# Kernel optimization log

Measured on AMD Instinct MI355X. Metric: run time of the kernel, lower is better.

## Reference

```python
import jax, jax.numpy as jnp
import numpy as np

B, S, D = 4, 2048, 1024
H = 16
HD = D // H


def setup_inputs() -> dict:
    key = jax.random.key(0)
    ks = jax.random.split(key, 5)
    scale = 0.02
    return {
        "x": jax.random.normal(ks[0], (B, S, D), dtype=jnp.float32),
        "wq": jax.random.normal(ks[1], (D, D), dtype=jnp.float32) * scale,
        "wk": jax.random.normal(ks[2], (D, D), dtype=jnp.float32) * scale,
        "wv": jax.random.normal(ks[3], (D, D), dtype=jnp.float32) * scale,
        "wo": jax.random.normal(ks[4], (D, D), dtype=jnp.float32) * scale,
    }


def reference(x, wq, wk, wv, wo):
    b, s, _ = x.shape
    # project and split heads: [b, h, s, hd]
    def proj(w):
        return jnp.einsum('bsd,de->bse', x, w).reshape(b, s, H, HD).transpose(0, 2, 1, 3)
    q, k, v = proj(wq), proj(wk), proj(wv)
    scores = jnp.einsum('bhqd,bhkd->bhqk', q, k)
    causal = jnp.tril(jnp.ones((s, s), dtype=bool))  # True = keep
    scores = jnp.where(causal, scores, -jnp.inf)
    attn = jax.nn.softmax(scores / jnp.sqrt(jnp.float32(HD)), axis=-1)
    ctx = jnp.einsum('bhqk,bhkd->bhqd', attn, v)
    ctx = ctx.transpose(0, 2, 1, 3).reshape(b, s, D)
    return jnp.einsum('bsd,de->bse', ctx, wo)
```

## Files before the change

kernel.cpp:

```cpp
#include <hip/hip_runtime.h>

#define S_LEN 2048
#define D_DIM 1024
#define NH    16
#define HD    64
#define BATCH 4
#define M_ROWS 8192

typedef __attribute__((ext_vector_type(8))) short bf16x8;
typedef __attribute__((ext_vector_type(4))) float f32x4;
typedef __attribute__((ext_vector_type(8))) unsigned short u16x8;

__device__ __forceinline__ unsigned short f2bf(float f) {
    unsigned u = __builtin_bit_cast(unsigned, f);
    u = (u + 0x7fffu + ((u >> 16) & 1u)) >> 16;
    return (unsigned short)u;
}
__device__ __forceinline__ unsigned pack2(float a, float b) {
    unsigned ua = __builtin_bit_cast(unsigned, a);
    unsigned ub = __builtin_bit_cast(unsigned, b);
    return ((ua + 0x8000u) >> 16) | ((ub + 0x8000u) & 0xffff0000u);
}

__device__ __forceinline__ void gload16(const void* g, void* l) {
    __builtin_amdgcn_global_load_lds((const __attribute__((address_space(1))) unsigned*)g,
                                     (__attribute__((address_space(3))) unsigned*)l,
                                     16, 0, 0);
}

__global__ __launch_bounds__(256) void prep_k(const float* __restrict__ x,
                                              const float* __restrict__ w0, const float* __restrict__ w1,
                                              const float* __restrict__ w2, const float* __restrict__ w3,
                                              unsigned short* __restrict__ xbf,
                                              unsigned short* __restrict__ o0, unsigned short* __restrict__ o1,
                                              unsigned short* __restrict__ o2, unsigned short* __restrict__ o3) {
    __shared__ float sT[64][65];
    const int t = threadIdx.x;
    if (blockIdx.x < 4096) {
        size_t i = (size_t)blockIdx.x * 256 + t;
        const float4* xf = (const float4*)x;
        float4 a = xf[2 * i], b = xf[2 * i + 1];
        u16x8 v;
        v[0] = f2bf(a.x); v[1] = f2bf(a.y); v[2] = f2bf(a.z); v[3] = f2bf(a.w);
        v[4] = f2bf(b.x); v[5] = f2bf(b.y); v[6] = f2bf(b.z); v[7] = f2bf(b.w);
        *(u16x8*)(xbf + i * 8) = v;
        return;
    }
    const int wb = blockIdx.x - 4096;
    const int z = wb >> 8;
    const float* w; unsigned short* o;
    switch (z) {
        case 0: w = w0; o = o0; break;
        case 1: w = w1; o = o1; break;
        case 2: w = w2; o = o2; break;
        default: w = w3; o = o3; break;
    }
    const float sc = (z == 0) ? 0.18033688011112042f : 1.0f;
    const int n0 = (wb & 15) * 64, k0 = ((wb >> 4) & 15) * 64;
    const int r = t >> 4, cq = t & 15;
#pragma unroll
    for (int it = 0; it < 4; ++it) {
        int k = r + it * 16;
        float4 v = *(const float4*)&w[(size_t)(k0 + k) * D_DIM + n0 + cq * 4];
        sT[k][cq * 4 + 0] = v.x; sT[k][cq * 4 + 1] = v.y;
        sT[k][cq * 4 + 2] = v.z; sT[k][cq * 4 + 3] = v.w;
    }
    __syncthreads();
    const int n = t >> 2, ch = t & 3;
    union { unsigned short s[8]; uint4 v; } p0, p1;
#pragma unroll
    for (int j = 0; j < 8; ++j) p0.s[j] = f2bf(sT[ch * 16 + j][n] * sc);
#pragma unroll
    for (int j = 0; j < 8; ++j) p1.s[j] = f2bf(sT[ch * 16 + 8 + j][n] * sc);
    *(uint4*)&o[(size_t)(n0 + n) * D_DIM + k0 + ch * 16]     = p0.v;
    *(uint4*)&o[(size_t)(n0 + n) * D_DIM + k0 + ch * 16 + 8] = p1.v;
}

__device__ __forceinline__ void gemm_core(const unsigned short* __restrict__ A,
                                          const unsigned short* __restrict__ Bt,
                                          unsigned short* sA, unsigned short* sB,
                                          int m0, int n0, int t, f32x4 acc[4][4])
{
    const int lane = t & 63, w = t >> 6;
    const int mm = lane & 15, quad = lane >> 4;
    const int wm = w >> 1, wn = w & 1;

    for (int k0 = 0; k0 < D_DIM; k0 += 64) {
        __syncthreads();
#pragma unroll
        for (int it = 0; it < 4; ++it) {
            int idx = t + it * 256;
            int m = idx >> 3, j = idx & 7;
            int g = j ^ (m & 7);
            gload16(A  + ((size_t)(m0 + m) * D_DIM + k0 + g * 8), (void*)&sA[idx * 8]);
            gload16(Bt + ((size_t)(n0 + m) * D_DIM + k0 + g * 8), (void*)&sB[idx * 8]);
        }
        __syncthreads();

#pragma unroll
        for (int kk = 0; kk < 2; ++kk) {
            bf16x8 af[4], bfr[4];
#pragma unroll
            for (int mi = 0; mi < 4; ++mi) {
                int m = wm * 64 + mi * 16 + mm;
                int slot = (kk * 4 + quad) ^ (m & 7);
                af[mi] = *(const bf16x8*)&sA[m * 64 + slot * 8];
            }
#pragma unroll
            for (int ni = 0; ni < 4; ++ni) {
                int n = wn * 64 + ni * 16 + mm;
                int slot = (kk * 4 + quad) ^ (n & 7);
                bfr[ni] = *(const bf16x8*)&sB[n * 64 + slot * 8];
            }
#pragma unroll
            for (int mi = 0; mi < 4; ++mi)
#pragma unroll
                for (int ni = 0; ni < 4; ++ni)
                    acc[mi][ni] = __builtin_amdgcn_mfma_f32_16x16x32_bf16(af[mi], bfr[ni], acc[mi][ni], 0, 0, 0);
        }
    }
}

__global__ __launch_bounds__(256) void gemmqkv_k(const unsigned short* __restrict__ A,
                                                 const unsigned short* __restrict__ Bt,
                                                 unsigned short* __restrict__ qb,
                                                 unsigned short* __restrict__ kb,
                                                 unsigned short* __restrict__ vt)
{
    __shared__ unsigned short sA[128 * 64];
    __shared__ unsigned short sB[128 * 64];
    const int t = threadIdx.x;
    const int lane = t & 63, w = t >> 6;
    const int mm = lane & 15, quad = lane >> 4;
    const int wm = w >> 1, wn = w & 1;
    const int m0 = blockIdx.y * 128, n0 = blockIdx.x * 128;

    f32x4 acc[4][4];
#pragma unroll
    for (int i = 0; i < 4; ++i)
#pragma unroll
        for (int j = 0; j < 4; ++j) acc[i][j] = (f32x4){0.f, 0.f, 0.f, 0.f};

    gemm_core(A, Bt, sA, sB, m0, n0, t, acc);

    const int widx = n0 >> 10;
    if (widx == 2) {
#pragma unroll
        for (int mi = 0; mi < 4; ++mi) {
            int rglob = m0 + wm * 64 + mi * 16 + quad * 4;
            int bb = rglob >> 11, ss = rglob & (S_LEN - 1);
#pragma unroll
            for (int ni = 0; ni < 4; ++ni) {
                int c = (n0 & 1023) + wn * 64 + ni * 16 + mm;
                int h = c >> 6, hd = c & 63;
                union { unsigned short s[4]; unsigned long long ll; } pk;
#pragma unroll
                for (int r = 0; r < 4; ++r) pk.s[r] = f2bf(acc[mi][ni][r]);
                *(unsigned long long*)&vt[((size_t)(bb * NH + h) * HD + hd) * S_LEN + ss] = pk.ll;
            }
        }
    } else {
        unsigned short* outp = widx ? kb : qb;
        const int nl0 = n0 & 1023;
#pragma unroll
        for (int mi = 0; mi < 4; ++mi)
#pragma unroll
            for (int ni = 0; ni < 4; ++ni)
#pragma unroll
                for (int r = 0; r < 4; ++r)
                    outp[(size_t)(m0 + wm * 64 + mi * 16 + quad * 4 + r) * D_DIM +
                         nl0 + wn * 64 + ni * 16 + mm] = f2bf(acc[mi][ni][r]);
    }
}

__global__ __launch_bounds__(256) void gemmo_k(const unsigned short* __restrict__ A,
                                               const unsigned short* __restrict__ Bt,
                                               float* __restrict__ C)
{
    __shared__ unsigned short sA[128 * 64];
    __shared__ unsigned short sB[128 * 64];
    const int t = threadIdx.x;
    const int lane = t & 63, w = t >> 6;
    const int mm = lane & 15, quad = lane >> 4;
    const int wm = w >> 1, wn = w & 1;
    const int m0 = blockIdx.y * 128, n0 = blockIdx.x * 128;

    f32x4 acc[4][4];
#pragma unroll
    for (int i = 0; i < 4; ++i)
#pragma unroll
        for (int j = 0; j < 4; ++j) acc[i][j] = (f32x4){0.f, 0.f, 0.f, 0.f};

    gemm_core(A, Bt, sA, sB, m0, n0, t, acc);

#pragma unroll
    for (int mi = 0; mi < 4; ++mi)
#pragma unroll
        for (int ni = 0; ni < 4; ++ni)
#pragma unroll
            for (int r = 0; r < 4; ++r)
                C[(size_t)(m0 + wm * 64 + mi * 16 + quad * 4 + r) * D_DIM +
                  n0 + wn * 64 + ni * 16 + mm] = acc[mi][ni][r];
}

__global__ __launch_bounds__(512, 4) void attn_k(const unsigned short* __restrict__ Q,
                                                 const unsigned short* __restrict__ K,
                                                 const unsigned short* __restrict__ Vt,
                                                 unsigned short* __restrict__ ctx)
{
    __shared__ unsigned short sK [2][64 * 64];
    __shared__ unsigned short sVT[2][64 * 64];
    __shared__ unsigned short sP [128 * 64];
    const int t = threadIdx.x;
    const int lane = t & 63, w = t >> 6;
    const int mm = lane & 15, quad = lane >> 4;
    const int pair = blockIdx.x, bh = blockIdx.y;
    const int b = bh >> 4, hh = bh & 15;
    const size_t rowbase = (size_t)b * S_LEN;
    const int coff = hh * HD;
    const unsigned short* Vh = Vt + (size_t)bh * HD * S_LEN;

    const int sc_ = t >> 3, sj = t & 7;
    const int sgk = sj ^ (sc_ & 7);

    u16x8 onesu;
#pragma unroll
    for (int j = 0; j < 8; ++j) onesu[j] = 0x3F80;
    const bf16x8 ones = __builtin_bit_cast(bf16x8, onesu);

    for (int sidx = 0; sidx < 2; ++sidx) {
        const int qt = sidx ? (15 - pair) : pair;
        const int q0 = qt * 128;

        bf16x8 qf[2];
#pragma unroll
        for (int kk = 0; kk < 2; ++kk)
            qf[kk] = *(const bf16x8*)(Q + (rowbase + q0 + w * 16 + mm) * D_DIM
                                        + coff + kk * 32 + quad * 8);
        f32x4 o[4], lacc;
        lacc = (f32x4){0.f, 0.f, 0.f, 0.f};
#pragma unroll
        for (int hf = 0; hf < 4; ++hf) o[hf] = (f32x4){0.f, 0.f, 0.f, 0.f};

        const int nkt = 2 * qt + 2;
        const int qr = q0 + w * 16 + mm;
        const int qrmax = q0 + w * 16 + 15;
        const int m = w * 16 + mm;

        gload16(K  + (rowbase + sc_) * D_DIM + coff + sgk * 8, (void*)&sK[0][t * 8]);
        gload16(Vh + (size_t)sc_ * S_LEN + sgk * 8,            (void*)&sVT[0][t * 8]);

        for (int kt = 0; kt < nkt; ++kt) {
            const int buf = kt & 1;
            __syncthreads();
            if (kt + 1 < nkt) {
                const int k1 = (kt + 1) * 64;
                gload16(K  + (rowbase + k1 + sc_) * D_DIM + coff + sgk * 8,
                        (void*)&sK[1 - buf][t * 8]);
                gload16(Vh + (size_t)sc_ * S_LEN + k1 + sgk * 8,
                        (void*)&sVT[1 - buf][t * 8]);
            }
            const int k0 = kt * 64;
            if (k0 > qrmax) continue;

            f32x4 sacc[4];
#pragma unroll
            for (int kf = 0; kf < 4; ++kf) sacc[kf] = (f32x4){0.f, 0.f, 0.f, 0.f};
#pragma unroll
            for (int kk = 0; kk < 2; ++kk) {
                bf16x8 ak[4];
#pragma unroll
                for (int kf = 0; kf < 4; ++kf) {
                    int key = kf * 16 + mm;
                    int slot = (kk * 4 + quad) ^ (key & 7);
                    ak[kf] = *(const bf16x8*)&sK[buf][key * 64 + slot * 8];
                }
#pragma unroll
                for (int kf = 0; kf < 4; ++kf)
                    sacc[kf] = __builtin_amdgcn_mfma_f32_16x16x32_bf16(ak[kf], qf[kk], sacc[kf], 0, 0, 0);
            }

            const bool needmask = (k0 + 63) > (q0 + w * 16);
#pragma unroll
            for (int kf = 0; kf < 4; ++kf) {
                float p[4];
#pragma unroll
                for (int r = 0; r < 4; ++r) {
                    p[r] = __builtin_amdgcn_exp2f(sacc[kf][r]);
                    if (needmask && (k0 + kf * 16 + quad * 4 + r) > qr) p[r] = 0.f;
                }
                unsigned lo = pack2(p[0], p[1]), hi = pack2(p[2], p[3]);
                int slot = (kf * 2 + (quad >> 1)) ^ (m & 7);
                *(unsigned long long*)&sP[m * 64 + slot * 8 + (quad & 1) * 4] =
                    ((unsigned long long)hi << 32) | lo;
            }

#pragma unroll
            for (int kk = 0; kk < 2; ++kk) {
                bf16x8 pf, vf[4];
                {
                    int slot = (kk * 4 + quad) ^ (m & 7);
                    pf = *(const bf16x8*)&sP[m * 64 + slot * 8];
                }
#pragma unroll
                for (int hf = 0; hf < 4; ++hf) {
                    int hd = hf * 16 + mm;
                    int slot = (kk * 4 + quad) ^ (hd & 7);
                    vf[hf] = *(const bf16x8*)&sVT[buf][hd * 64 + slot * 8];
                }
                lacc = __builtin_amdgcn_mfma_f32_16x16x32_bf16(pf, ones, lacc, 0, 0, 0);
#pragma unroll
                for (int hf = 0; hf < 4; ++hf)
                    o[hf] = __builtin_amdgcn_mfma_f32_16x16x32_bf16(pf, vf[hf], o[hf], 0, 0, 0);
            }
        }
        __syncthreads();

#pragma unroll
        for (int r = 0; r < 4; ++r) {
            float inv = 1.f / lacc[r];
            int row = q0 + w * 16 + quad * 4 + r;
#pragma unroll
            for (int hf = 0; hf < 4; ++hf)
                ctx[(rowbase + row) * D_DIM + coff + hf * 16 + mm] = f2bf(o[hf][r] * inv);
        }
    }
}

extern "C" void kernel_launch(void* const* d_in, const int* in_sizes, int n_in,
                              void* d_out, int out_size, void* d_ws, size_t ws_size,
                              hipStream_t stream)
{
    const float* x  = (const float*)d_in[0];
    const float* wq = (const float*)d_in[1];
    const float* wk = (const float*)d_in[2];
    const float* wv = (const float*)d_in[3];
    const float* wo = (const float*)d_in[4];

    const size_t XE = (size_t)M_ROWS * D_DIM;
    const size_t WE = (size_t)D_DIM * D_DIM;
    unsigned short* ws  = (unsigned short*)d_ws;
    unsigned short* xbf = ws;
    unsigned short* wt0 = xbf + XE;
    unsigned short* wt1 = wt0 + WE;
    unsigned short* wt2 = wt1 + WE;
    unsigned short* wt3 = wt2 + WE;
    unsigned short* qb  = wt3 + WE;
    unsigned short* kb  = qb + XE;
    unsigned short* vt  = kb + XE;
    unsigned short* cb  = vt + XE;

    prep_k<<<dim3(4096 + 1024), 256, 0, stream>>>(x, wq, wk, wv, wo,
                                                  xbf, wt0, wt1, wt2, wt3);

    gemmqkv_k<<<dim3(3 * D_DIM / 128, M_ROWS / 128), 256, 0, stream>>>(xbf, wt0, qb, kb, vt);

    attn_k<<<dim3(8, BATCH * NH), 512, 0, stream>>>(qb, kb, vt, cb);

    gemmo_k<<<dim3(D_DIM / 128, M_ROWS / 128), 256, 0, stream>>>(cb, wt3, (float*)d_out);
}
```

Before: 250.8 us.

## Pipeline GEMM loads with a 4-stage LDS ring and 128x256 tiles

Rewrites the shared GEMM core used by the QKV and output projections as a 4-deep asynchronous global-to-LDS ring with a K-step of 32. Loads are issued three tiles ahead and consumption is gated with explicit vmcnt waits and barriers, so memory latency overlaps MFMA work instead of serialising behind a barrier every iteration. Tiles grow to 128x256 with 512 threads and 8 waves, and MFMA issue gets raised priority. The trade-off is more LDS per block (96 KB), fewer blocks in the grid, and fragile hand-counted vmcnt values.

```diff
diff --git a/kernel.cpp b/kernel.cpp
--- a/kernel.cpp
+++ b/kernel.cpp
@@ -26,6 +26,14 @@
     __builtin_amdgcn_global_load_lds((const __attribute__((address_space(1))) unsigned*)g,
                                      (__attribute__((address_space(3))) unsigned*)l,
                                      16, 0, 0);
+}
+
+template<int N> __device__ __forceinline__ void vmwait() {
+    static_assert(N == 0 || N == 3 || N == 6 || N == 9, "unexpected vmcnt");
+    if constexpr (N == 0) asm volatile("s_waitcnt vmcnt(0)" ::: "memory");
+    if constexpr (N == 3) asm volatile("s_waitcnt vmcnt(3)" ::: "memory");
+    if constexpr (N == 6) asm volatile("s_waitcnt vmcnt(6)" ::: "memory");
+    if constexpr (N == 9) asm volatile("s_waitcnt vmcnt(9)" ::: "memory");
 }
 
 __global__ __launch_bounds__(256) void prep_k(const float* __restrict__ x,
@@ -76,74 +84,125 @@
     *(uint4*)&o[(size_t)(n0 + n) * D_DIM + k0 + ch * 16 + 8] = p1.v;
 }
 
-__device__ __forceinline__ void gemm_core(const unsigned short* __restrict__ A,
+static constexpr int GBM = 128;
+static constexpr int GBN = 256;
+static constexpr int GNT = 32;
+
+__device__ __forceinline__ void gemm_pipe(const unsigned short* __restrict__ A,
                                           const unsigned short* __restrict__ Bt,
                                           unsigned short* sA, unsigned short* sB,
-                                          int m0, int n0, int t, f32x4 acc[4][4])
+                                          int m0, int n0, int t,
+                                          f32x4 (&acc)[4][4])
 {
     const int lane = t & 63, w = t >> 6;
     const int mm = lane & 15, quad = lane >> 4;
-    const int wm = w >> 1, wn = w & 1;
-
-    for (int k0 = 0; k0 < D_DIM; k0 += 64) {
-        __syncthreads();
-#pragma unroll
-        for (int it = 0; it < 4; ++it) {
-            int idx = t + it * 256;
-            int m = idx >> 3, j = idx & 7;
-            int g = j ^ (m & 7);
-            gload16(A  + ((size_t)(m0 + m) * D_DIM + k0 + g * 8), (void*)&sA[idx * 8]);
-            gload16(Bt + ((size_t)(n0 + m) * D_DIM + k0 + g * 8), (void*)&sB[idx * 8]);
+    const int wm = w >> 2, wn = w & 3;
+
+    const unsigned short* asrc;
+    {
+        int r = t >> 2, j = t & 3, g = j ^ ((r >> 1) & 3);
+        asrc = A + (size_t)(m0 + r) * D_DIM + g * 8;
+    }
+    const unsigned short* bsrc[2];
+#pragma unroll
+    for (int i = 0; i < 2; ++i) {
+        int r = i * 128 + (t >> 2), j = t & 3, g = j ^ ((r >> 1) & 3);
+        bsrc[i] = Bt + (size_t)(n0 + r) * D_DIM + g * 8;
+    }
+
+    auto stage = [&](int buf, int kt) {
+        const int ko = kt * 32;
+        gload16(asrc + ko, sA + buf * (GBM * 32) + t * 8);
+#pragma unroll
+        for (int i = 0; i < 2; ++i)
+            gload16(bsrc[i] + ko, sB + buf * (GBN * 32) + i * 4096 + t * 8);
+    };
+
+    auto compute = [&](int buf) {
+        bf16x8 af[4], bfr[4];
+#pragma unroll
+        for (int mi = 0; mi < 4; ++mi) {
+            int m = wm * 64 + mi * 16 + mm;
+            int slot = quad ^ ((m >> 1) & 3);
+            af[mi] = *(const bf16x8*)&sA[buf * (GBM * 32) + m * 32 + slot * 8];
         }
-        __syncthreads();
-
-#pragma unroll
-        for (int kk = 0; kk < 2; ++kk) {
-            bf16x8 af[4], bfr[4];
-#pragma unroll
-            for (int mi = 0; mi < 4; ++mi) {
-                int m = wm * 64 + mi * 16 + mm;
-                int slot = (kk * 4 + quad) ^ (m & 7);
-                af[mi] = *(const bf16x8*)&sA[m * 64 + slot * 8];
-            }
-#pragma unroll
-            for (int ni = 0; ni < 4; ++ni) {
-                int n = wn * 64 + ni * 16 + mm;
-                int slot = (kk * 4 + quad) ^ (n & 7);
-                bfr[ni] = *(const bf16x8*)&sB[n * 64 + slot * 8];
-            }
-#pragma unroll
-            for (int mi = 0; mi < 4; ++mi)
-#pragma unroll
-                for (int ni = 0; ni < 4; ++ni)
-                    acc[mi][ni] = __builtin_amdgcn_mfma_f32_16x16x32_bf16(af[mi], bfr[ni], acc[mi][ni], 0, 0, 0);
+#pragma unroll
+        for (int ni = 0; ni < 4; ++ni) {
+            int n = wn * 64 + ni * 16 + mm;
+            int slot = quad ^ ((n >> 1) & 3);
+            bfr[ni] = *(const bf16x8*)&sB[buf * (GBN * 32) + n * 32 + slot * 8];
         }
-    }
-}
-
-__global__ __launch_bounds__(256) void gemmqkv_k(const unsigned short* __restrict__ A,
-                                                 const unsigned short* __restrict__ Bt,
-                                                 unsigned short* __restrict__ qb,
-                                                 unsigned short* __restrict__ kb,
-                                                 unsigned short* __restrict__ vt)
+        __builtin_amdgcn_s_setprio(1);
+#pragma unroll
+        for (int mi = 0; mi < 4; ++mi)
+#pragma unroll
+            for (int ni = 0; ni < 4; ++ni)
+                acc[mi][ni] = __builtin_amdgcn_mfma_f32_16x16x32_bf16(af[mi], bfr[ni], acc[mi][ni], 0, 0, 0);
+        __builtin_amdgcn_s_setprio(0);
+    };
+
+#pragma unroll
+    for (int tt = 0; tt < 3; ++tt) stage(tt, tt);
+
+#pragma unroll 4
+    for (int kt = 0; kt < 28; ++kt) {
+        stage((kt + 3) & 3, kt + 3);
+        vmwait<9>();
+        __builtin_amdgcn_s_barrier();
+        asm volatile("" ::: "memory");
+        compute(kt & 3);
+        asm volatile("s_waitcnt lgkmcnt(0)" ::: "memory");
+        __builtin_amdgcn_s_barrier();
+    }
+    stage(3, 31);
+    vmwait<9>();
+    __builtin_amdgcn_s_barrier();
+    asm volatile("" ::: "memory");
+    compute(0);
+    asm volatile("s_waitcnt lgkmcnt(0)" ::: "memory");
+    __builtin_amdgcn_s_barrier();
+    vmwait<6>();
+    __builtin_amdgcn_s_barrier();
+    asm volatile("" ::: "memory");
+    compute(1);
+    asm volatile("s_waitcnt lgkmcnt(0)" ::: "memory");
+    __builtin_amdgcn_s_barrier();
+    vmwait<3>();
+    __builtin_amdgcn_s_barrier();
+    asm volatile("" ::: "memory");
+    compute(2);
+    asm volatile("s_waitcnt lgkmcnt(0)" ::: "memory");
+    __builtin_amdgcn_s_barrier();
+    vmwait<0>();
+    __builtin_amdgcn_s_barrier();
+    asm volatile("" ::: "memory");
+    compute(3);
+}
+
+__global__ __launch_bounds__(512, 2) void gemmqkv_k(const unsigned short* __restrict__ A,
+                                                    const unsigned short* __restrict__ Bt,
+                                                    unsigned short* __restrict__ qb,
+                                                    unsigned short* __restrict__ kb,
+                                                    unsigned short* __restrict__ vt)
 {
-    __shared__ unsigned short sA[128 * 64];
-    __shared__ unsigned short sB[128 * 64];
+    __shared__ unsigned short sA[4 * GBM * 32];
+    __shared__ unsigned short sB[4 * GBN * 32];
     const int t = threadIdx.x;
+    const int m0 = blockIdx.y * GBM, n0 = blockIdx.x * GBN;
+
+    f32x4 acc[4][4];
+#pragma unroll
+    for (int i = 0; i < 4; ++i)
+#pragma unroll
+        for (int j = 0; j < 4; ++j) acc[i][j] = (f32x4){0.f, 0.f, 0.f, 0.f};
+
+    gemm_pipe(A, Bt, sA, sB, m0, n0, t, acc);
+
     const int lane = t & 63, w = t >> 6;
     const int mm = lane & 15, quad = lane >> 4;
-    const int wm = w >> 1, wn = w & 1;
-    const int m0 = blockIdx.y * 128, n0 = blockIdx.x * 128;
-
-    f32x4 acc[4][4];
-#pragma unroll
-    for (int i = 0; i < 4; ++i)
-#pragma unroll
-        for (int j = 0; j < 4; ++j) acc[i][j] = (f32x4){0.f, 0.f, 0.f, 0.f};
-
-    gemm_core(A, Bt, sA, sB, m0, n0, t, acc);
-
-    const int widx = n0 >> 10;
+    const int wm = w >> 2, wn = w & 3;
+    const int widx = n0 >> 10, nl0 = n0 & 1023;
+
     if (widx == 2) {
 #pragma unroll
         for (int mi = 0; mi < 4; ++mi) {
@@ -151,7 +210,7 @@
             int bb = rglob >> 11, ss = rglob & (S_LEN - 1);
 #pragma unroll
             for (int ni = 0; ni < 4; ++ni) {
-                int c = (n0 & 1023) + wn * 64 + ni * 16 + mm;
+                int c = nl0 + wn * 64 + ni * 16 + mm;
                 int h = c >> 6, hd = c & 63;
                 union { unsigned short s[4]; unsigned long long ll; } pk;
 #pragma unroll
@@ -161,7 +220,6 @@
         }
     } else {
         unsigned short* outp = widx ? kb : qb;
-        const int nl0 = n0 & 1023;
 #pragma unroll
         for (int mi = 0; mi < 4; ++mi)
 #pragma unroll
@@ -173,25 +231,26 @@
     }
 }
 
-__global__ __launch_bounds__(256) void gemmo_k(const unsigned short* __restrict__ A,
-                                               const unsigned short* __restrict__ Bt,
-                                               float* __restrict__ C)
+__global__ __launch_bounds__(512, 2) void gemmo_k(const unsigned short* __restrict__ A,
+                                                  const unsigned short* __restrict__ Bt,
+                                                  float* __restrict__ C)
 {
-    __shared__ unsigned short sA[128 * 64];
-    __shared__ unsigned short sB[128 * 64];
+    __shared__ unsigned short sA[4 * GBM * 32];
+    __shared__ unsigned short sB[4 * GBN * 32];
     const int t = threadIdx.x;
+    const int m0 = blockIdx.y * GBM, n0 = blockIdx.x * GBN;
+
+    f32x4 acc[4][4];
+#pragma unroll
+    for (int i = 0; i < 4; ++i)
+#pragma unroll
+        for (int j = 0; j < 4; ++j) acc[i][j] = (f32x4){0.f, 0.f, 0.f, 0.f};
+
+    gemm_pipe(A, Bt, sA, sB, m0, n0, t, acc);
+
     const int lane = t & 63, w = t >> 6;
     const int mm = lane & 15, quad = lane >> 4;
-    const int wm = w >> 1, wn = w & 1;
-    const int m0 = blockIdx.y * 128, n0 = blockIdx.x * 128;
-
-    f32x4 acc[4][4];
-#pragma unroll
-    for (int i = 0; i < 4; ++i)
-#pragma unroll
-        for (int j = 0; j < 4; ++j) acc[i][j] = (f32x4){0.f, 0.f, 0.f, 0.f};
-
-    gemm_core(A, Bt, sA, sB, m0, n0, t, acc);
+    const int wm = w >> 2, wn = w & 3;
 
 #pragma unroll
     for (int mi = 0; mi < 4; ++mi)
@@ -353,9 +412,9 @@
     prep_k<<<dim3(4096 + 1024), 256, 0, stream>>>(x, wq, wk, wv, wo,
                                                   xbf, wt0, wt1, wt2, wt3);
 
-    gemmqkv_k<<<dim3(3 * D_DIM / 128, M_ROWS / 128), 256, 0, stream>>>(xbf, wt0, qb, kb, vt);
+    gemmqkv_k<<<dim3(3 * D_DIM / GBN, M_ROWS / GBM), 512, 0, stream>>>(xbf, wt0, qb, kb, vt);
 
     attn_k<<<dim3(8, BATCH * NH), 512, 0, stream>>>(qb, kb, vt, cb);
 
-    gemmo_k<<<dim3(D_DIM / 128, M_ROWS / 128), 256, 0, stream>>>(cb, wt3, (float*)d_out);
-}
+    gemmo_k<<<dim3(D_DIM / GBN, M_ROWS / GBM), 512, 0, stream>>>(cb, wt3, (float*)d_out);
+}
```

Measured after the change: 263.5 us. +5.1%, slower.

## Rewrite projection GEMMs as 256x256 tiles with 4-stage async LDS pipeline

Applied to the files above, without the earlier changes.

Both projection GEMMs move from 128x128 tiles with a load-then-compute loop per k-step to 256x256 tiles computed by 8 waves. The new loop is a fully unrolled 4-slot ring buffer that prefetches three k-steps ahead, uses explicit vmcnt waits and barriers, and raises wave priority around MFMA blocks. Workgroup IDs are remapped for XCD-aware scheduling. The aim is to hide global load latency and improve data reuse, at the cost of more registers, more LDS per block, and fewer blocks in flight (128 for the output GEMM, fewer than the CU count).

```diff
diff --git a/kernel.cpp b/kernel.cpp
--- a/kernel.cpp
+++ b/kernel.cpp
@@ -76,131 +76,199 @@
     *(uint4*)&o[(size_t)(n0 + n) * D_DIM + k0 + ch * 16 + 8] = p1.v;
 }
 
-__device__ __forceinline__ void gemm_core(const unsigned short* __restrict__ A,
-                                          const unsigned short* __restrict__ Bt,
-                                          unsigned short* sA, unsigned short* sB,
-                                          int m0, int n0, int t, f32x4 acc[4][4])
+static constexpr int BM = 256, BN = 256, BK = 32;
+
+#define TILE_STEP(T_, WN_, ST_)                                                         \
+{                                                                                       \
+    const int slot_ = (T_) & 3;                                                         \
+    const unsigned so_ = (unsigned)slot_ * 8192u;                                       \
+    bf16x8 af_[4], bv_[4];                                                              \
+    _Pragma("unroll")                                                                   \
+    for (int nf = 0; nf < 4; ++nf)                                                      \
+        bv_[nf] = *(const bf16x8*)&sB[so_ + bh * 4096 + (bl + nf * 16) * 32 + xs * 8];  \
+    _Pragma("unroll")                                                                   \
+    for (int mf = 0; mf < 4; ++mf)                                                      \
+        af_[mf] = *(const bf16x8*)&sA[so_ + (al + mf * 16) * 32 + xs * 8];              \
+    if (ST_) {                                                                          \
+        const int ko_ = ((T_) + 3) * 32;                                                \
+        const unsigned wd_ = (unsigned)(((T_) + 3) & 3) * 8192u;                        \
+        gload16(a0 + ko_, dA + wd_);                                                    \
+        gload16(b0 + ko_, dB + wd_);                                                    \
+    }                                                                                   \
+    __builtin_amdgcn_s_barrier();                                                       \
+    asm volatile("s_waitcnt lgkmcnt(0)" ::: "memory");                                  \
+    __builtin_amdgcn_s_setprio(1);                                                      \
+    _Pragma("unroll")                                                                   \
+    for (int mf = 0; mf < 4; ++mf)                                                      \
+        _Pragma("unroll")                                                               \
+        for (int nf = 0; nf < 4; ++nf)                                                  \
+            acc[0][mf][nf] = __builtin_amdgcn_mfma_f32_16x16x32_bf16(af_[mf], bv_[nf], acc[0][mf][nf], 0, 0, 0); \
+    __builtin_amdgcn_s_setprio(0);                                                      \
+    __builtin_amdgcn_s_barrier();                                                       \
+    _Pragma("unroll")                                                                   \
+    for (int mf = 0; mf < 4; ++mf)                                                      \
+        af_[mf] = *(const bf16x8*)&sA[so_ + 4096 + (al + mf * 16) * 32 + xs * 8];       \
+    if (ST_) {                                                                          \
+        const int ko_ = ((T_) + 3) * 32;                                                \
+        const unsigned wd_ = (unsigned)(((T_) + 3) & 3) * 8192u;                        \
+        gload16(a1 + ko_, dA + wd_ + 4096);                                             \
+        gload16(b1 + ko_, dB + wd_ + 4096);                                             \
+    }                                                                                   \
+    __builtin_amdgcn_s_barrier();                                                       \
+    asm volatile("s_waitcnt lgkmcnt(0)" ::: "memory");                                  \
+    __builtin_amdgcn_s_setprio(1);                                                      \
+    _Pragma("unroll")                                                                   \
+    for (int mf = 0; mf < 4; ++mf)                                                      \
+        _Pragma("unroll")                                                               \
+        for (int nf = 0; nf < 4; ++nf)                                                  \
+            acc[1][mf][nf] = __builtin_amdgcn_mfma_f32_16x16x32_bf16(af_[mf], bv_[nf], acc[1][mf][nf], 0, 0, 0); \
+    __builtin_amdgcn_s_setprio(0);                                                      \
+    if ((WN_) == 8)      asm volatile("s_waitcnt vmcnt(8)" ::: "memory");               \
+    else if ((WN_) == 4) asm volatile("s_waitcnt vmcnt(4)" ::: "memory");               \
+    else if ((WN_) == 0) asm volatile("s_waitcnt vmcnt(0)" ::: "memory");               \
+    __builtin_amdgcn_s_barrier();                                                       \
+}
+
+__device__ __forceinline__ void gemm256(const unsigned short* __restrict__ A,
+                                        const unsigned short* __restrict__ Bt,
+                                        unsigned short* sA, unsigned short* sB,
+                                        int m0, int n0, int t,
+                                        f32x4 (&acc)[2][4][4])
 {
-    const int lane = t & 63, w = t >> 6;
+    const int lane = t & 63, wid = t >> 6;
     const int mm = lane & 15, quad = lane >> 4;
-    const int wm = w >> 1, wn = w & 1;
-
-    for (int k0 = 0; k0 < D_DIM; k0 += 64) {
-        __syncthreads();
-#pragma unroll
-        for (int it = 0; it < 4; ++it) {
-            int idx = t + it * 256;
-            int m = idx >> 3, j = idx & 7;
-            int g = j ^ (m & 7);
-            gload16(A  + ((size_t)(m0 + m) * D_DIM + k0 + g * 8), (void*)&sA[idx * 8]);
-            gload16(Bt + ((size_t)(n0 + m) * D_DIM + k0 + g * 8), (void*)&sB[idx * 8]);
-        }
-        __syncthreads();
-
-#pragma unroll
-        for (int kk = 0; kk < 2; ++kk) {
-            bf16x8 af[4], bfr[4];
-#pragma unroll
-            for (int mi = 0; mi < 4; ++mi) {
-                int m = wm * 64 + mi * 16 + mm;
-                int slot = (kk * 4 + quad) ^ (m & 7);
-                af[mi] = *(const bf16x8*)&sA[m * 64 + slot * 8];
-            }
+    const int wm = wid >> 2, wn = wid & 3;
+
+    const int sr = t >> 2;
+    const int sg = (t & 3) ^ ((sr >> 1) & 3);
+    const unsigned short* a0 = A  + (size_t)(m0 + sr) * D_DIM + sg * 8;
+    const unsigned short* a1 = a0 + 128 * D_DIM;
+    const unsigned short* b0 = Bt + (size_t)(n0 + sr) * D_DIM + sg * 8;
+    const unsigned short* b1 = b0 + 128 * D_DIM;
+    unsigned short* dA = sA + t * 8;
+    unsigned short* dB = sB + t * 8;
+
+    const int al = wm * 64 + mm;
+    const int bl = (wn & 1) * 64 + mm;
+    const int bh = wn >> 1;
+    const int xs = quad ^ ((mm >> 1) & 3);
+
+#pragma unroll
+    for (int pt = 0; pt < 3; ++pt) {
+        const int ko = pt * 32;
+        const unsigned wd = (unsigned)pt * 8192u;
+        gload16(a0 + ko, dA + wd);
+        gload16(b0 + ko, dB + wd);
+        gload16(a1 + ko, dA + wd + 4096);
+        gload16(b1 + ko, dB + wd + 4096);
+    }
+    asm volatile("s_waitcnt vmcnt(8)" ::: "memory");
+    __builtin_amdgcn_s_barrier();
+
+    for (int T = 0; T < 28; ++T) TILE_STEP(T, 8, true);
+    TILE_STEP(28, 8, true);
+    TILE_STEP(29, 4, false);
+    TILE_STEP(30, 0, false);
+    TILE_STEP(31, -1, false);
+}
+
+__global__ __launch_bounds__(512, 2) void gemmqkv_k(const unsigned short* __restrict__ A,
+                                                    const unsigned short* __restrict__ Bt,
+                                                    unsigned short* __restrict__ qb,
+                                                    unsigned short* __restrict__ kb,
+                                                    unsigned short* __restrict__ vt)
+{
+    __shared__ unsigned short sA[4 * 2 * 128 * 32];
+    __shared__ unsigned short sB[4 * 2 * 128 * 32];
+    const int t = threadIdx.x;
+    const int bid = blockIdx.x;
+    const int wg = (bid & 7) * 48 + (bid >> 3);
+    const int mt = wg / 12, nt = wg % 12;
+    const int m0 = mt * BM, n0 = nt * BN;
+
+    f32x4 acc[2][4][4];
+#pragma unroll
+    for (int q = 0; q < 2; ++q)
+#pragma unroll
+        for (int i = 0; i < 4; ++i)
+#pragma unroll
+            for (int j = 0; j < 4; ++j) acc[q][i][j] = (f32x4){0.f, 0.f, 0.f, 0.f};
+
+    gemm256(A, Bt, sA, sB, m0, n0, t, acc);
+
+    const int lane = t & 63, wid = t >> 6;
+    const int mm = lane & 15, quad = lane >> 4;
+    const int wm = wid >> 2, wn = wid & 3;
+    const int widx = n0 >> 10, nl0 = n0 & 1023;
+
+    if (widx == 2) {
+#pragma unroll
+        for (int qm = 0; qm < 2; ++qm)
+#pragma unroll
+        for (int mi = 0; mi < 4; ++mi) {
+            int rglob = m0 + qm * 128 + wm * 64 + mi * 16 + quad * 4;
+            int bb = rglob >> 11, ss = rglob & (S_LEN - 1);
 #pragma unroll
             for (int ni = 0; ni < 4; ++ni) {
-                int n = wn * 64 + ni * 16 + mm;
-                int slot = (kk * 4 + quad) ^ (n & 7);
-                bfr[ni] = *(const bf16x8*)&sB[n * 64 + slot * 8];
-            }
-#pragma unroll
-            for (int mi = 0; mi < 4; ++mi)
-#pragma unroll
-                for (int ni = 0; ni < 4; ++ni)
-                    acc[mi][ni] = __builtin_amdgcn_mfma_f32_16x16x32_bf16(af[mi], bfr[ni], acc[mi][ni], 0, 0, 0);
-        }
-    }
-}
-
-__global__ __launch_bounds__(256) void gemmqkv_k(const unsigned short* __restrict__ A,
-                                                 const unsigned short* __restrict__ Bt,
-                                                 unsigned short* __restrict__ qb,
-                                                 unsigned short* __restrict__ kb,
-                                                 unsigned short* __restrict__ vt)
-{
-    __shared__ unsigned short sA[128 * 64];
-    __shared__ unsigned short sB[128 * 64];
-    const int t = threadIdx.x;
-    const int lane = t & 63, w = t >> 6;
-    const int mm = lane & 15, quad = lane >> 4;
-    const int wm = w >> 1, wn = w & 1;
-    const int m0 = blockIdx.y * 128, n0 = blockIdx.x * 128;
-
-    f32x4 acc[4][4];
-#pragma unroll
-    for (int i = 0; i < 4; ++i)
-#pragma unroll
-        for (int j = 0; j < 4; ++j) acc[i][j] = (f32x4){0.f, 0.f, 0.f, 0.f};
-
-    gemm_core(A, Bt, sA, sB, m0, n0, t, acc);
-
-    const int widx = n0 >> 10;
-    if (widx == 2) {
-#pragma unroll
-        for (int mi = 0; mi < 4; ++mi) {
-            int rglob = m0 + wm * 64 + mi * 16 + quad * 4;
-            int bb = rglob >> 11, ss = rglob & (S_LEN - 1);
-#pragma unroll
-            for (int ni = 0; ni < 4; ++ni) {
-                int c = (n0 & 1023) + wn * 64 + ni * 16 + mm;
+                int c = nl0 + wn * 64 + ni * 16 + mm;
                 int h = c >> 6, hd = c & 63;
                 union { unsigned short s[4]; unsigned long long ll; } pk;
 #pragma unroll
-                for (int r = 0; r < 4; ++r) pk.s[r] = f2bf(acc[mi][ni][r]);
+                for (int r = 0; r < 4; ++r) pk.s[r] = f2bf(acc[qm][mi][ni][r]);
                 *(unsigned long long*)&vt[((size_t)(bb * NH + h) * HD + hd) * S_LEN + ss] = pk.ll;
             }
         }
     } else {
         unsigned short* outp = widx ? kb : qb;
-        const int nl0 = n0 & 1023;
+#pragma unroll
+        for (int qm = 0; qm < 2; ++qm)
 #pragma unroll
         for (int mi = 0; mi < 4; ++mi)
 #pragma unroll
             for (int ni = 0; ni < 4; ++ni)
 #pragma unroll
                 for (int r = 0; r < 4; ++r)
-                    outp[(size_t)(m0 + wm * 64 + mi * 16 + quad * 4 + r) * D_DIM +
-                         nl0 + wn * 64 + ni * 16 + mm] = f2bf(acc[mi][ni][r]);
-    }
-}
-
-__global__ __launch_bounds__(256) void gemmo_k(const unsigned short* __restrict__ A,
-                                               const unsigned short* __restrict__ Bt,
-                                               float* __restrict__ C)
+                    outp[(size_t)(m0 + qm * 128 + wm * 64 + mi * 16 + quad * 4 + r) * D_DIM +
+                         nl0 + wn * 64 + ni * 16 + mm] = f2bf(acc[qm][mi][ni][r]);
+    }
+}
+
+__global__ __launch_bounds__(512, 2) void gemmo_k(const unsigned short* __restrict__ A,
+                                                  const unsigned short* __restrict__ Bt,
+                                                  float* __restrict__ C)
 {
-    __shared__ unsigned short sA[128 * 64];
-    __shared__ unsigned short sB[128 * 64];
+    __shared__ unsigned short sA[4 * 2 * 128 * 32];
+    __shared__ unsigned short sB[4 * 2 * 128 * 32];
     const int t = threadIdx.x;
-    const int lane = t & 63, w = t >> 6;
+    const int bid = blockIdx.x;
+    const int wg = (bid & 7) * 16 + (bid >> 3);
+    const int mt = wg >> 2, nt = wg & 3;
+    const int m0 = mt * BM, n0 = nt * BN;
+
+    f32x4 acc[2][4][4];
+#pragma unroll
+    for (int q = 0; q < 2; ++q)
+#pragma unroll
+        for (int i = 0; i < 4; ++i)
+#pragma unroll
+            for (int j = 0; j < 4; ++j) acc[q][i][j] = (f32x4){0.f, 0.f, 0.f, 0.f};
+
+    gemm256(A, Bt, sA, sB, m0, n0, t, acc);
+
+    const int lane = t & 63, wid = t >> 6;
     const int mm = lane & 15, quad = lane >> 4;
-    const int wm = w >> 1, wn = w & 1;
-    const int m0 = blockIdx.y * 128, n0 = blockIdx.x * 128;
-
-    f32x4 acc[4][4];
-#pragma unroll
-    for (int i = 0; i < 4; ++i)
-#pragma unroll
-        for (int j = 0; j < 4; ++j) acc[i][j] = (f32x4){0.f, 0.f, 0.f, 0.f};
-
-    gemm_core(A, Bt, sA, sB, m0, n0, t, acc);
-
+    const int wm = wid >> 2, wn = wid & 3;
+
+#pragma unroll
+    for (int qm = 0; qm < 2; ++qm)
 #pragma unroll
     for (int mi = 0; mi < 4; ++mi)
 #pragma unroll
         for (int ni = 0; ni < 4; ++ni)
 #pragma unroll
             for (int r = 0; r < 4; ++r)
-                C[(size_t)(m0 + wm * 64 + mi * 16 + quad * 4 + r) * D_DIM +
-                  n0 + wn * 64 + ni * 16 + mm] = acc[mi][ni][r];
+                C[(size_t)(m0 + qm * 128 + wm * 64 + mi * 16 + quad * 4 + r) * D_DIM +
+                  n0 + wn * 64 + ni * 16 + mm] = acc[qm][mi][ni][r];
 }
 
 __global__ __launch_bounds__(512, 4) void attn_k(const unsigned short* __restrict__ Q,
@@ -353,9 +421,9 @@
     prep_k<<<dim3(4096 + 1024), 256, 0, stream>>>(x, wq, wk, wv, wo,
                                                   xbf, wt0, wt1, wt2, wt3);
 
-    gemmqkv_k<<<dim3(3 * D_DIM / 128, M_ROWS / 128), 256, 0, stream>>>(xbf, wt0, qb, kb, vt);
+    gemmqkv_k<<<dim3(384), 512, 0, stream>>>(xbf, wt0, qb, kb, vt);
 
     attn_k<<<dim3(8, BATCH * NH), 512, 0, stream>>>(qb, kb, vt, cb);
 
-    gemmo_k<<<dim3(D_DIM / 128, M_ROWS / 128), 256, 0, stream>>>(cb, wt3, (float*)d_out);
-}
+    gemmo_k<<<dim3(128), 512, 0, stream>>>(cb, wt3, (float*)d_out);
+}
```

Result: slower. 263.2 us (+4.9%).

## Rewrite projection GEMMs with 4-stage LDS pipeline, larger tiles, XCD-aware block mapping

Applied to the files above, without the earlier changes.

Rewrites the shared GEMM core to use a 4-slot ring of K=32 LDS stages filled with global_load_lds, with explicit vmcnt waits and a single barrier per step in place of two syncs per K-step. Workgroups grow to 512 threads with 128x384 tiles for QKV and 128x256 for the output projection. Block IDs are remapped so that consecutive tiles go to the same XCD, and MFMA issue gets a raised priority. The aim is to hide global load latency and reduce synchronisation and redundant A-tile loads, at the cost of more LDS per block and lower occupancy.

```diff
diff --git a/kernel.cpp b/kernel.cpp
--- a/kernel.cpp
+++ b/kernel.cpp
@@ -26,6 +26,14 @@
     __builtin_amdgcn_global_load_lds((const __attribute__((address_space(1))) unsigned*)g,
                                      (__attribute__((address_space(3))) unsigned*)l,
                                      16, 0, 0);
+}
+
+template<int N> __device__ __forceinline__ void vmwait() {
+    if constexpr (N == 0)      asm volatile("s_waitcnt vmcnt(0)" ::: "memory");
+    else if constexpr (N == 3) asm volatile("s_waitcnt vmcnt(3)" ::: "memory");
+    else if constexpr (N == 4) asm volatile("s_waitcnt vmcnt(4)" ::: "memory");
+    else if constexpr (N == 6) asm volatile("s_waitcnt vmcnt(6)" ::: "memory");
+    else if constexpr (N == 8) asm volatile("s_waitcnt vmcnt(8)" ::: "memory");
 }
 
 __global__ __launch_bounds__(256) void prep_k(const float* __restrict__ x,
@@ -76,131 +84,167 @@
     *(uint4*)&o[(size_t)(n0 + n) * D_DIM + k0 + ch * 16 + 8] = p1.v;
 }
 
+template<int NFRAG, int NGLD>
 __device__ __forceinline__ void gemm_core(const unsigned short* __restrict__ A,
                                           const unsigned short* __restrict__ Bt,
-                                          unsigned short* sA, unsigned short* sB,
-                                          int m0, int n0, int t, f32x4 acc[4][4])
+                                          unsigned short* __restrict__ sA,
+                                          unsigned short* __restrict__ sB,
+                                          int m0, int n0, int t,
+                                          f32x4 (&acc)[4][NFRAG])
 {
-    const int lane = t & 63, w = t >> 6;
+    constexpr int BSLOT = (NGLD - 1) * 4096;
+    const int lane = t & 63, wid = t >> 6;
     const int mm = lane & 15, quad = lane >> 4;
-    const int wm = w >> 1, wn = w & 1;
-
-    for (int k0 = 0; k0 < D_DIM; k0 += 64) {
-        __syncthreads();
-#pragma unroll
-        for (int it = 0; it < 4; ++it) {
-            int idx = t + it * 256;
-            int m = idx >> 3, j = idx & 7;
-            int g = j ^ (m & 7);
-            gload16(A  + ((size_t)(m0 + m) * D_DIM + k0 + g * 8), (void*)&sA[idx * 8]);
-            gload16(Bt + ((size_t)(n0 + m) * D_DIM + k0 + g * 8), (void*)&sB[idx * 8]);
-        }
-        __syncthreads();
-
-#pragma unroll
-        for (int kk = 0; kk < 2; ++kk) {
-            bf16x8 af[4], bfr[4];
-#pragma unroll
-            for (int mi = 0; mi < 4; ++mi) {
-                int m = wm * 64 + mi * 16 + mm;
-                int slot = (kk * 4 + quad) ^ (m & 7);
-                af[mi] = *(const bf16x8*)&sA[m * 64 + slot * 8];
-            }
-#pragma unroll
-            for (int ni = 0; ni < 4; ++ni) {
-                int n = wn * 64 + ni * 16 + mm;
-                int slot = (kk * 4 + quad) ^ (n & 7);
-                bfr[ni] = *(const bf16x8*)&sB[n * 64 + slot * 8];
-            }
-#pragma unroll
-            for (int mi = 0; mi < 4; ++mi)
-#pragma unroll
-                for (int ni = 0; ni < 4; ++ni)
-                    acc[mi][ni] = __builtin_amdgcn_mfma_f32_16x16x32_bf16(af[mi], bfr[ni], acc[mi][ni], 0, 0, 0);
-        }
-    }
-}
-
-__global__ __launch_bounds__(256) void gemmqkv_k(const unsigned short* __restrict__ A,
-                                                 const unsigned short* __restrict__ Bt,
-                                                 unsigned short* __restrict__ qb,
-                                                 unsigned short* __restrict__ kb,
-                                                 unsigned short* __restrict__ vt)
+    const int wm = wid >> 2, wn = wid & 3;
+
+    const int sr = t >> 2;
+    const int sg = (t & 3) ^ ((sr >> 1) & 3);
+    const unsigned short* asrc  = A  + (size_t)(m0 + sr) * D_DIM + sg * 8;
+    const unsigned short* bsrc0 = Bt + (size_t)(n0 + sr) * D_DIM + sg * 8;
+    unsigned short* dA = sA + t * 8;
+    unsigned short* dB = sB + t * 8;
+
+    const int al = wm * 64 + mm;
+    const int bl = wn * (NFRAG * 16) + mm;
+    const int xs = quad ^ ((mm >> 1) & 3);
+
+#pragma unroll
+    for (int pt = 0; pt < 3; ++pt) {
+        const int ko = pt * 32;
+        gload16(asrc + ko, dA + pt * 4096);
+#pragma unroll
+        for (int p = 0; p < NGLD - 1; ++p)
+            gload16(bsrc0 + (size_t)p * 128 * D_DIM + ko, dB + pt * BSLOT + p * 4096);
+    }
+    vmwait<2 * NGLD>();
+    __builtin_amdgcn_s_barrier();
+
+#define GTILE(T_, W_, ST_)                                                                 \
+{                                                                                          \
+    const unsigned soA_ = (unsigned)((T_) & 3) * 4096u;                                    \
+    const unsigned soB_ = (unsigned)((T_) & 3) * (unsigned)BSLOT;                          \
+    if (ST_) {                                                                             \
+        const int ko_ = ((T_) + 3) * 32;                                                   \
+        const unsigned wA_ = (unsigned)(((T_) + 3) & 3) * 4096u;                           \
+        const unsigned wB_ = (unsigned)(((T_) + 3) & 3) * (unsigned)BSLOT;                 \
+        gload16(asrc + ko_, dA + wA_);                                                     \
+        _Pragma("unroll")                                                                  \
+        for (int p_ = 0; p_ < NGLD - 1; ++p_)                                              \
+            gload16(bsrc0 + (size_t)p_ * 128 * D_DIM + ko_, dB + wB_ + p_ * 4096);         \
+    }                                                                                      \
+    bf16x8 af_[4], bv_[NFRAG];                                                             \
+    _Pragma("unroll")                                                                      \
+    for (int nf = 0; nf < NFRAG; ++nf)                                                     \
+        bv_[nf] = *(const bf16x8*)&sB[soB_ + (unsigned)(bl + nf * 16) * 32 + xs * 8];      \
+    _Pragma("unroll")                                                                      \
+    for (int mf = 0; mf < 4; ++mf)                                                         \
+        af_[mf] = *(const bf16x8*)&sA[soA_ + (unsigned)(al + mf * 16) * 32 + xs * 8];      \
+    asm volatile("s_waitcnt lgkmcnt(0)" ::: "memory");                                     \
+    __builtin_amdgcn_s_setprio(1);                                                         \
+    _Pragma("unroll")                                                                      \
+    for (int mf = 0; mf < 4; ++mf)                                                         \
+        _Pragma("unroll")                                                                  \
+        for (int nf = 0; nf < NFRAG; ++nf)                                                 \
+            acc[mf][nf] = __builtin_amdgcn_mfma_f32_16x16x32_bf16(af_[mf], bv_[nf], acc[mf][nf], 0, 0, 0); \
+    __builtin_amdgcn_s_setprio(0);                                                         \
+    vmwait<(W_)>();                                                                        \
+    __builtin_amdgcn_s_barrier();                                                          \
+}
+
+#pragma unroll 4
+    for (int T = 0; T < 28; ++T) GTILE(T, 2 * NGLD, true);
+    GTILE(28, 2 * NGLD, true);
+    GTILE(29, NGLD, false);
+    GTILE(30, 0, false);
+    GTILE(31, -1, false);
+#undef GTILE
+}
+
+__global__ __launch_bounds__(512, 2) void gemmqkv_k(const unsigned short* __restrict__ A,
+                                                    const unsigned short* __restrict__ Bt,
+                                                    unsigned short* __restrict__ qb,
+                                                    unsigned short* __restrict__ kb,
+                                                    unsigned short* __restrict__ vt)
 {
-    __shared__ unsigned short sA[128 * 64];
-    __shared__ unsigned short sB[128 * 64];
+    __shared__ unsigned short sA[4 * 4096];
+    __shared__ unsigned short sB[4 * 3 * 4096];
     const int t = threadIdx.x;
-    const int lane = t & 63, w = t >> 6;
+    const int bid = blockIdx.x;
+    const int wg = (bid & 7) * 64 + (bid >> 3);
+    const int mt = wg >> 3, nt = wg & 7;
+    const int m0 = mt * 128, n0 = nt * 384;
+
+    f32x4 acc[4][6];
+#pragma unroll
+    for (int i = 0; i < 4; ++i)
+#pragma unroll
+        for (int j = 0; j < 6; ++j) acc[i][j] = (f32x4){0.f, 0.f, 0.f, 0.f};
+
+    gemm_core<6, 4>(A, Bt, sA, sB, m0, n0, t, acc);
+
+    const int lane = t & 63, wid = t >> 6;
     const int mm = lane & 15, quad = lane >> 4;
-    const int wm = w >> 1, wn = w & 1;
-    const int m0 = blockIdx.y * 128, n0 = blockIdx.x * 128;
-
-    f32x4 acc[4][4];
-#pragma unroll
-    for (int i = 0; i < 4; ++i)
-#pragma unroll
-        for (int j = 0; j < 4; ++j) acc[i][j] = (f32x4){0.f, 0.f, 0.f, 0.f};
-
-    gemm_core(A, Bt, sA, sB, m0, n0, t, acc);
-
-    const int widx = n0 >> 10;
-    if (widx == 2) {
-#pragma unroll
-        for (int mi = 0; mi < 4; ++mi) {
-            int rglob = m0 + wm * 64 + mi * 16 + quad * 4;
-            int bb = rglob >> 11, ss = rglob & (S_LEN - 1);
-#pragma unroll
-            for (int ni = 0; ni < 4; ++ni) {
-                int c = (n0 & 1023) + wn * 64 + ni * 16 + mm;
-                int h = c >> 6, hd = c & 63;
+    const int wm = wid >> 2, wn = wid & 3;
+
+#pragma unroll
+    for (int nf = 0; nf < 6; ++nf) {
+        const int c0 = n0 + wn * 96 + nf * 16;
+        const int widx = c0 >> 10, nl0 = c0 & 1023;
+        if (widx == 2) {
+            const int h = nl0 >> 6, hd = (nl0 & 63) + mm;
+#pragma unroll
+            for (int mf = 0; mf < 4; ++mf) {
+                int rglob = m0 + wm * 64 + mf * 16 + quad * 4;
+                int bb = rglob >> 11, ss = rglob & (S_LEN - 1);
                 union { unsigned short s[4]; unsigned long long ll; } pk;
 #pragma unroll
-                for (int r = 0; r < 4; ++r) pk.s[r] = f2bf(acc[mi][ni][r]);
+                for (int r = 0; r < 4; ++r) pk.s[r] = f2bf(acc[mf][nf][r]);
                 *(unsigned long long*)&vt[((size_t)(bb * NH + h) * HD + hd) * S_LEN + ss] = pk.ll;
             }
+        } else {
+            unsigned short* outp = widx ? kb : qb;
+#pragma unroll
+            for (int mf = 0; mf < 4; ++mf)
+#pragma unroll
+                for (int r = 0; r < 4; ++r)
+                    outp[(size_t)(m0 + wm * 64 + mf * 16 + quad * 4 + r) * D_DIM +
+                         nl0 + mm] = f2bf(acc[mf][nf][r]);
         }
-    } else {
-        unsigned short* outp = widx ? kb : qb;
-        const int nl0 = n0 & 1023;
-#pragma unroll
-        for (int mi = 0; mi < 4; ++mi)
-#pragma unroll
-            for (int ni = 0; ni < 4; ++ni)
-#pragma unroll
-                for (int r = 0; r < 4; ++r)
-                    outp[(size_t)(m0 + wm * 64 + mi * 16 + quad * 4 + r) * D_DIM +
-                         nl0 + wn * 64 + ni * 16 + mm] = f2bf(acc[mi][ni][r]);
-    }
-}
-
-__global__ __launch_bounds__(256) void gemmo_k(const unsigned short* __restrict__ A,
-                                               const unsigned short* __restrict__ Bt,
-                                               float* __restrict__ C)
+    }
+}
+
+__global__ __launch_bounds__(512, 2) void gemmo_k(const unsigned short* __restrict__ A,
+                                                  const unsigned short* __restrict__ Bt,
+                                                  float* __restrict__ C)
 {
-    __shared__ unsigned short sA[128 * 64];
-    __shared__ unsigned short sB[128 * 64];
+    __shared__ unsigned short sA[4 * 4096];
+    __shared__ unsigned short sB[4 * 2 * 4096];
     const int t = threadIdx.x;
-    const int lane = t & 63, w = t >> 6;
+    const int bid = blockIdx.x;
+    const int wg = (bid & 7) * 32 + (bid >> 3);
+    const int mt = wg >> 2, nt = wg & 3;
+    const int m0 = mt * 128, n0 = nt * 256;
+
+    f32x4 acc[4][4];
+#pragma unroll
+    for (int i = 0; i < 4; ++i)
+#pragma unroll
+        for (int j = 0; j < 4; ++j) acc[i][j] = (f32x4){0.f, 0.f, 0.f, 0.f};
+
+    gemm_core<4, 3>(A, Bt, sA, sB, m0, n0, t, acc);
+
+    const int lane = t & 63, wid = t >> 6;
     const int mm = lane & 15, quad = lane >> 4;
-    const int wm = w >> 1, wn = w & 1;
-    const int m0 = blockIdx.y * 128, n0 = blockIdx.x * 128;
-
-    f32x4 acc[4][4];
-#pragma unroll
-    for (int i = 0; i < 4; ++i)
-#pragma unroll
-        for (int j = 0; j < 4; ++j) acc[i][j] = (f32x4){0.f, 0.f, 0.f, 0.f};
-
-    gemm_core(A, Bt, sA, sB, m0, n0, t, acc);
-
-#pragma unroll
-    for (int mi = 0; mi < 4; ++mi)
-#pragma unroll
-        for (int ni = 0; ni < 4; ++ni)
+    const int wm = wid >> 2, wn = wid & 3;
+
+#pragma unroll
+    for (int mf = 0; mf < 4; ++mf)
+#pragma unroll
+        for (int nf = 0; nf < 4; ++nf)
 #pragma unroll
             for (int r = 0; r < 4; ++r)
-                C[(size_t)(m0 + wm * 64 + mi * 16 + quad * 4 + r) * D_DIM +
-                  n0 + wn * 64 + ni * 16 + mm] = acc[mi][ni][r];
+                C[(size_t)(m0 + wm * 64 + mf * 16 + quad * 4 + r) * D_DIM +
+                  n0 + wn * 64 + nf * 16 + mm] = acc[mf][nf][r];
 }
 
 __global__ __launch_bounds__(512, 4) void attn_k(const unsigned short* __restrict__ Q,
@@ -353,9 +397,9 @@
     prep_k<<<dim3(4096 + 1024), 256, 0, stream>>>(x, wq, wk, wv, wo,
                                                   xbf, wt0, wt1, wt2, wt3);
 
-    gemmqkv_k<<<dim3(3 * D_DIM / 128, M_ROWS / 128), 256, 0, stream>>>(xbf, wt0, qb, kb, vt);
+    gemmqkv_k<<<dim3(512), 512, 0, stream>>>(xbf, wt0, qb, kb, vt);
 
     attn_k<<<dim3(8, BATCH * NH), 512, 0, stream>>>(qb, kb, vt, cb);
 
-    gemmo_k<<<dim3(D_DIM / 128, M_ROWS / 128), 256, 0, stream>>>(cb, wt3, (float*)d_out);
-}
+    gemmo_k<<<dim3(256), 512, 0, stream>>>(cb, wt3, (float*)d_out);
+}
```

New measurement: 252.3 us. About the same (+0.6%).
